# Performance work log

Hardware: AMD Instinct MI355X
Metric: run time of the kernel (lower is better)

## Reference

```python
import jax, jax.numpy as jnp
import numpy as np

B, L, H, E = 16, 1024, 8, 64
S, D = L, E
TOKEN_NUM = L


def setup_inputs() -> dict:
    key = jax.random.key(0)
    kq, kk, kv, kw = jax.random.split(key, 4)
    queries = jax.random.normal(kq, (B, L, H, E), dtype=jnp.float32)
    keys = jax.random.normal(kk, (B, S, H, E), dtype=jnp.float32)
    values = jax.random.normal(kv, (B, S, H, D), dtype=jnp.float32)
    # init as in module: eye + randn, shaped [1, num_heads=1, T, T]
    weight_mat = (jnp.eye(TOKEN_NUM, dtype=jnp.float32)
                  + jax.random.normal(kw, (TOKEN_NUM, TOKEN_NUM), dtype=jnp.float32))[None, None]
    tau = jnp.ones((1, 1, TOKEN_NUM, 1), dtype=jnp.float32)
    attn_mask = jnp.zeros((1,), dtype=bool)  # unused (mask_flag=False)
    return {"queries": queries, "keys": keys, "values": values,
            "weight_mat": weight_mat, "tau": tau, "attn_mask": attn_mask}


def reference(queries, keys, values, weight_mat, tau, attn_mask):
    # queries: [B,L,H,E], keys: [B,S,H,E], values: [B,S,H,D]
    scale = 1.0 / jnp.sqrt(jnp.asarray(queries.shape[-1], queries.dtype))
    scores = jnp.einsum('blhe,bshe->bhls', queries, keys) * scale  # [B,H,L,S]
    # learned modulation: softmax(weight_mat / softplus(tau)) over last dim
    w = jax.nn.softmax(weight_mat / jax.nn.softplus(tau), axis=-1)  # [1,1,L,S]
    A = jax.nn.softmax(scores * w, axis=-1)  # inside-softmax multiplicative path
    # dropout is identity in eval mode
    V = jnp.einsum('bhls,bshd->blhd', A, values)  # [B,L,H,D]
    return V
```

## Files before the change

kernel.cpp:

```cpp
#include <hip/hip_runtime.h>

using short8 = __attribute__((ext_vector_type(8))) short;
using f32x16 = __attribute__((ext_vector_type(16))) float;

__device__ __forceinline__ short b16(float f) {
  __bf16 h = (__bf16)f;
  return __builtin_bit_cast(short, h);
}
__device__ __forceinline__ short8 pack8(const float4& a, const float4& b) {
  short8 r;
  r[0] = b16(a.x); r[1] = b16(a.y); r[2] = b16(a.z); r[3] = b16(a.w);
  r[4] = b16(b.x); r[5] = b16(b.y); r[6] = b16(b.z); r[7] = b16(b.w);
  return r;
}
__device__ __forceinline__ unsigned pk2(float lo, float hi) {
  return ((unsigned)(unsigned short)b16(hi) << 16) | (unsigned)(unsigned short)b16(lo);
}

__global__ __launch_bounds__(256) void w_softmax_kernel(
    const float* __restrict__ wm, const float* __restrict__ tau,
    float* __restrict__ wout) {
  const int row = blockIdx.x;
  const int tid = threadIdx.x;
  const float sp  = log1pf(__expf(tau[row]));
  const float inv = 1.0f / sp;
  const float4* src = (const float4*)(wm + (size_t)row * 1024);
  float4 v = src[tid];
  float v0 = v.x * inv, v1 = v.y * inv, v2 = v.z * inv, v3 = v.w * inv;
  float mx = fmaxf(fmaxf(v0, v1), fmaxf(v2, v3));
  #pragma unroll
  for (int m = 1; m < 64; m <<= 1) mx = fmaxf(mx, __shfl_xor(mx, m));
  __shared__ float red[8];
  const int wv = tid >> 6;
  if ((tid & 63) == 0) red[wv] = mx;
  __syncthreads();
  mx = fmaxf(fmaxf(red[0], red[1]), fmaxf(red[2], red[3]));
  float e0 = __expf(v0 - mx), e1 = __expf(v1 - mx);
  float e2 = __expf(v2 - mx), e3 = __expf(v3 - mx);
  float s = e0 + e1 + e2 + e3;
  #pragma unroll
  for (int m = 1; m < 64; m <<= 1) s += __shfl_xor(s, m);
  if ((tid & 63) == 0) red[4 + wv] = s;
  __syncthreads();
  s = red[4] + red[5] + red[6] + red[7];
  const float r = 0.125f / s;
  float4* dst = (float4*)(wout + (size_t)row * 1024);
  float4 o; o.x = e0 * r; o.y = e1 * r; o.z = e2 * r; o.w = e3 * r;
  dst[tid] = o;
}

__global__ __launch_bounds__(256, 2) void attn_kernel(
    const float* __restrict__ Q, const float* __restrict__ K,
    const float* __restrict__ V, const float* __restrict__ W,
    float* __restrict__ O) {
  const int orig = blockIdx.x;
  const int bid  = (orig & 7) * 128 + (orig >> 3);
  const int qblk = bid >> 7;
  const int bh   = bid & 127;
  const int b = bh >> 3, h = bh & 7;

  const int tid = threadIdx.x, wv = tid >> 6, lane = tid & 63;
  const int ql = lane & 31, hi = lane >> 5;
  const int qg = qblk * 128 + wv * 32 + ql;

  __shared__ alignas(16) short Ks[2][4096];
  __shared__ alignas(16) short Vt[2][4096];
  __shared__ float Sc[128];

  const float* qrow = Q + ((size_t)(b * 1024 + qg)) * 512 + h * 64;
  short8 qb[4];
  #pragma unroll
  for (int es = 0; es < 4; ++es) {
    float4 f0 = *(const float4*)(qrow + es * 16 + hi * 8);
    float4 f1 = *(const float4*)(qrow + es * 16 + hi * 8 + 4);
    qb[es] = pack8(f0, f1);
  }

  const int srow = tid >> 2;
  const int cgrp = (tid & 3) * 16;
  const float* kp = K + ((size_t)(b * 1024 + srow)) * 512 + h * 64 + cgrp;
  const float* vp = V + ((size_t)(b * 1024 + srow)) * 512 + h * 64 + cgrp;
  const int kswz = (srow & 7) << 4;
  const int kwb0 = srow * 128 + ((cgrp * 2) ^ kswz);
  const int kwb1 = srow * 128 + ((cgrp * 2 + 16) ^ kswz);

  {
    float4 a0 = *(const float4*)(kp);
    float4 a1 = *(const float4*)(kp + 4);
    float4 a2 = *(const float4*)(kp + 8);
    float4 a3 = *(const float4*)(kp + 12);
    float4 c0 = *(const float4*)(vp);
    float4 c1 = *(const float4*)(vp + 4);
    float4 c2 = *(const float4*)(vp + 8);
    float4 c3 = *(const float4*)(vp + 12);
    *(short8*)((char*)Ks[0] + kwb0) = pack8(a0, a1);
    *(short8*)((char*)Ks[0] + kwb1) = pack8(a2, a3);
    float va[16] = {c0.x, c0.y, c0.z, c0.w, c1.x, c1.y, c1.z, c1.w,
                    c2.x, c2.y, c2.z, c2.w, c3.x, c3.y, c3.z, c3.w};
    #pragma unroll
    for (int j = 0; j < 16; ++j) {
      const int d = cgrp + j;
      const int vswz = (((d & 7) ^ (d >> 3)) & 7) << 4;
      *(short*)((char*)Vt[0] + d * 128 + ((srow * 2) ^ vswz)) = b16(va[j]);
    }
  }
  __syncthreads();

  f32x16 o0, o1;
  #pragma unroll
  for (int i = 0; i < 16; ++i) { o0[i] = 0.f; o1[i] = 0.f; }
  float m_r = -INFINITY, l_r = 0.f;

  const float* wr = W + (size_t)qg * 1024;

  #pragma unroll 1
  for (int kt = 0; kt < 16; ++kt) {
    const int c = kt & 1;
    const int s0 = kt * 64;

    float4 nk0, nk1, nk2, nk3, nv0, nv1, nv2, nv3;
    if (kt < 15) {
      const size_t soff = (size_t)((kt + 1) * 64) * 512;
      nk0 = *(const float4*)(kp + soff);      nk1 = *(const float4*)(kp + soff + 4);
      nk2 = *(const float4*)(kp + soff + 8);  nk3 = *(const float4*)(kp + soff + 12);
      nv0 = *(const float4*)(vp + soff);      nv1 = *(const float4*)(vp + soff + 4);
      nv2 = *(const float4*)(vp + soff + 8);  nv3 = *(const float4*)(vp + soff + 12);
    }

    float wreg[32];
    #pragma unroll
    for (int st = 0; st < 2; ++st)
      #pragma unroll
      for (int rg = 0; rg < 4; ++rg) {
        float4 t = *(const float4*)(wr + s0 + st * 32 + rg * 8 + hi * 4);
        wreg[st * 16 + rg * 4 + 0] = t.x;
        wreg[st * 16 + rg * 4 + 1] = t.y;
        wreg[st * 16 + rg * 4 + 2] = t.z;
        wreg[st * 16 + rg * 4 + 3] = t.w;
      }

    f32x16 sa0, sa1;
    #pragma unroll
    for (int i = 0; i < 16; ++i) { sa0[i] = 0.f; sa1[i] = 0.f; }
    {
      const int sr0 = ql, sr1 = 32 + ql;
      const char* kb0 = (const char*)Ks[c] + sr0 * 128;
      const char* kb1 = (const char*)Ks[c] + sr1 * 128;
      const int sz0 = (sr0 & 7) << 4, sz1 = (sr1 & 7) << 4;
      #pragma unroll
      for (int es = 0; es < 4; ++es) {
        short8 ka0 = *(const short8*)(kb0 + ((es * 32 + hi * 16) ^ sz0));
        short8 ka1 = *(const short8*)(kb1 + ((es * 32 + hi * 16) ^ sz1));
        sa0 = __builtin_amdgcn_mfma_f32_32x32x16_bf16(ka0, qb[es], sa0, 0, 0, 0);
        sa1 = __builtin_amdgcn_mfma_f32_32x32x16_bf16(ka1, qb[es], sa1, 0, 0, 0);
      }
    }

    float lg[32];
    #pragma unroll
    for (int reg = 0; reg < 16; ++reg) {
      lg[reg]      = sa0[reg] * wreg[reg];
      lg[16 + reg] = sa1[reg] * wreg[16 + reg];
    }

    float t16[16];
    #pragma unroll
    for (int i = 0; i < 16; ++i) t16[i] = fmaxf(lg[i], lg[i + 16]);
    float t8[8];
    #pragma unroll
    for (int i = 0; i < 8; ++i) t8[i] = fmaxf(t16[i], t16[i + 8]);
    float t4[4];
    #pragma unroll
    for (int i = 0; i < 4; ++i) t4[i] = fmaxf(t8[i], t8[i + 4]);
    float pmax = fmaxf(fmaxf(t4[0], t4[1]), fmaxf(t4[2], t4[3]));
    pmax = fmaxf(pmax, __shfl_xor(pmax, 32));

    if (!__all(pmax <= m_r + 8.0f)) {
      const float mnew = fmaxf(m_r, pmax);
      const float corr = __expf(m_r - mnew);
      m_r = mnew;
      l_r *= corr;
      if (lane < 32) Sc[wv * 32 + ql] = corr;
      #pragma unroll
      for (int reg = 0; reg < 16; ++reg) {
        const float cr = Sc[wv * 32 + ((reg & 3) + 8 * (reg >> 2) + 4 * hi)];
        o0[reg] *= cr; o1[reg] *= cr;
      }
    }

    float p[32];
    #pragma unroll
    for (int i = 0; i < 32; ++i) p[i] = __expf(lg[i] - m_r);
    float s16[16];
    #pragma unroll
    for (int i = 0; i < 16; ++i) s16[i] = p[i] + p[i + 16];
    float s8[8];
    #pragma unroll
    for (int i = 0; i < 8; ++i) s8[i] = s16[i] + s16[i + 8];
    float s4[4];
    #pragma unroll
    for (int i = 0; i < 4; ++i) s4[i] = s8[i] + s8[i + 4];
    float rs = (s4[0] + s4[1]) + (s4[2] + s4[3]);
    rs += __shfl_xor(rs, 32);
    l_r += rs;

    unsigned cc[16];
    #pragma unroll
    for (int t = 0; t < 16; ++t) cc[t] = pk2(p[2 * t], p[2 * t + 1]);
    short8 pa[4];
    #pragma unroll
    for (int ks = 0; ks < 4; ++ks) {
      unsigned snd0 = hi ? cc[4 * ks]     : cc[4 * ks + 2];
      unsigned snd1 = hi ? cc[4 * ks + 1] : cc[4 * ks + 3];
      unsigned e0 = __shfl_xor(snd0, 32);
      unsigned e1 = __shfl_xor(snd1, 32);
      uint4 dw;
      dw.x = hi ? e0 : cc[4 * ks];
      dw.y = hi ? e1 : cc[4 * ks + 1];
      dw.z = hi ? cc[4 * ks + 2] : e0;
      dw.w = hi ? cc[4 * ks + 3] : e1;
      pa[ks] = __builtin_bit_cast(short8, dw);
    }

    #pragma unroll
    for (int nt = 0; nt < 2; ++nt) {
      const int d = nt * 32 + ql;
      const char* vb = (const char*)Vt[c] + d * 128;
      const int vswz = (((d & 7) ^ (d >> 3)) & 7) << 4;
      #pragma unroll
      for (int ks = 0; ks < 4; ++ks) {
        short8 bf = *(const short8*)(vb + ((ks * 32 + hi * 16) ^ vswz));
        if (nt == 0) o0 = __builtin_amdgcn_mfma_f32_32x32x16_bf16(pa[ks], bf, o0, 0, 0, 0);
        else         o1 = __builtin_amdgcn_mfma_f32_32x32x16_bf16(pa[ks], bf, o1, 0, 0, 0);
      }
    }

    if (kt < 15) {
      *(short8*)((char*)Ks[c ^ 1] + kwb0) = pack8(nk0, nk1);
      *(short8*)((char*)Ks[c ^ 1] + kwb1) = pack8(nk2, nk3);
      float va[16] = {nv0.x, nv0.y, nv0.z, nv0.w, nv1.x, nv1.y, nv1.z, nv1.w,
                      nv2.x, nv2.y, nv2.z, nv2.w, nv3.x, nv3.y, nv3.z, nv3.w};
      #pragma unroll
      for (int j = 0; j < 16; ++j) {
        const int d = cgrp + j;
        const int vswz = (((d & 7) ^ (d >> 3)) & 7) << 4;
        *(short*)((char*)Vt[c ^ 1] + d * 128 + ((srow * 2) ^ vswz)) = b16(va[j]);
      }
    }
    __syncthreads();
  }

  if (lane < 32) Sc[wv * 32 + ql] = l_r;
  #pragma unroll
  for (int reg = 0; reg < 16; ++reg) {
    const int qq = (reg & 3) + 8 * (reg >> 2) + 4 * hi;
    const float lv = Sc[wv * 32 + qq];
    const float inv = 1.0f / lv;
    float* op = O + ((size_t)(b * 1024 + qblk * 128 + wv * 32 + qq)) * 512 + h * 64 + ql;
    op[0]  = o0[reg] * inv;
    op[32] = o1[reg] * inv;
  }
}

extern "C" void kernel_launch(void* const* d_in, const int* in_sizes, int n_in,
                              void* d_out, int out_size, void* d_ws, size_t ws_size,
                              hipStream_t stream) {
  const float* Q   = (const float*)d_in[0];
  const float* K   = (const float*)d_in[1];
  const float* V   = (const float*)d_in[2];
  const float* WM  = (const float*)d_in[3];
  const float* TAU = (const float*)d_in[4];
  float* Wbuf = (float*)d_ws;
  float* out  = (float*)d_out;

  w_softmax_kernel<<<dim3(1024), dim3(256), 0, stream>>>(WM, TAU, Wbuf);
  attn_kernel<<<dim3(1024), dim3(256), 0, stream>>>(Q, K, V, Wbuf, out);
}
```

Measured before the change: 254.7 us.

## Store modulation weights as transposed bf16, remap blocks per XCD, raise MFMA priority

The softmaxed weight matrix is now written in bf16 and a new kernel transposes it, so the attention kernel reads each score's weight as a 16-bit value from a column-major layout. The block-to-work mapping changes so every XCD handles 16 batch-heads across all query blocks, and s_setprio is raised around the MFMA sections. The intent is to halve the weight traffic and improve L2 locality of K/V per XCD. The costs are an extra kernel launch and bf16 rounding of the weights. Each lane now issues 32 scalar 2-byte loads strided by 1024 elements, which could coalesce poorly.

```diff
diff --git a/kernel.cpp b/kernel.cpp
--- a/kernel.cpp
+++ b/kernel.cpp
@@ -16,10 +16,13 @@
 __device__ __forceinline__ unsigned pk2(float lo, float hi) {
   return ((unsigned)(unsigned short)b16(hi) << 16) | (unsigned)(unsigned short)b16(lo);
 }
+__device__ __forceinline__ float bf2f(unsigned short u) {
+  return __builtin_bit_cast(float, ((unsigned)u) << 16);
+}
 
 __global__ __launch_bounds__(256) void w_softmax_kernel(
     const float* __restrict__ wm, const float* __restrict__ tau,
-    float* __restrict__ wout) {
+    unsigned short* __restrict__ wout) {
   const int row = blockIdx.x;
   const int tid = threadIdx.x;
   const float sp  = log1pf(__expf(tau[row]));
@@ -44,19 +47,44 @@
   __syncthreads();
   s = red[4] + red[5] + red[6] + red[7];
   const float r = 0.125f / s;
-  float4* dst = (float4*)(wout + (size_t)row * 1024);
-  float4 o; o.x = e0 * r; o.y = e1 * r; o.z = e2 * r; o.w = e3 * r;
-  dst[tid] = o;
+  ushort4 o;
+  o.x = (unsigned short)b16(e0 * r); o.y = (unsigned short)b16(e1 * r);
+  o.z = (unsigned short)b16(e2 * r); o.w = (unsigned short)b16(e3 * r);
+  *(ushort4*)(wout + (size_t)row * 1024 + tid * 4) = o;
+}
+
+__global__ __launch_bounds__(256) void w_transpose_kernel(
+    const unsigned short* __restrict__ win, unsigned short* __restrict__ wt) {
+  __shared__ unsigned short tile[64][73];
+  const int ti = blockIdx.x & 15;
+  const int tj = blockIdx.x >> 4;
+  const int t  = threadIdx.x;
+  const int qa = t >> 2;
+  const int sb = (t & 3) * 16;
+  const unsigned short* src = win + (size_t)(tj * 64 + qa) * 1024 + ti * 64 + sb;
+  short8 a0 = *(const short8*)(src);
+  short8 a1 = *(const short8*)(src + 8);
+  #pragma unroll
+  for (int j = 0; j < 8; ++j) { tile[qa][sb + j] = a0[j]; tile[qa][sb + 8 + j] = a1[j]; }
+  __syncthreads();
+  const int sr = t >> 2;
+  const int qb = (t & 3) * 16;
+  short8 w0, w1;
+  #pragma unroll
+  for (int j = 0; j < 8; ++j) { w0[j] = tile[qb + j][sr]; w1[j] = tile[qb + 8 + j][sr]; }
+  unsigned short* dst = wt + (size_t)(ti * 64 + sr) * 1024 + tj * 64 + qb;
+  *(short8*)(dst) = w0;
+  *(short8*)(dst + 8) = w1;
 }
 
 __global__ __launch_bounds__(256, 2) void attn_kernel(
     const float* __restrict__ Q, const float* __restrict__ K,
-    const float* __restrict__ V, const float* __restrict__ W,
+    const float* __restrict__ V, const unsigned short* __restrict__ Wt,
     float* __restrict__ O) {
   const int orig = blockIdx.x;
-  const int bid  = (orig & 7) * 128 + (orig >> 3);
-  const int qblk = bid >> 7;
-  const int bh   = bid & 127;
+  const int xcd  = orig & 7, slot = orig >> 3;
+  const int bh   = xcd * 16 + (slot >> 3);
+  const int qblk = slot & 7;
   const int b = bh >> 3, h = bh & 7;
 
   const int tid = threadIdx.x, wv = tid >> 6, lane = tid & 63;
@@ -111,7 +139,7 @@
   for (int i = 0; i < 16; ++i) { o0[i] = 0.f; o1[i] = 0.f; }
   float m_r = -INFINITY, l_r = 0.f;
 
-  const float* wr = W + (size_t)qg * 1024;
+  const unsigned short* wcol = Wt + qg;
 
   #pragma unroll 1
   for (int kt = 0; kt < 16; ++kt) {
@@ -127,17 +155,15 @@
       nv2 = *(const float4*)(vp + soff + 8);  nv3 = *(const float4*)(vp + soff + 12);
     }
 
-    float wreg[32];
+    unsigned short wu[32];
     #pragma unroll
     for (int st = 0; st < 2; ++st)
       #pragma unroll
-      for (int rg = 0; rg < 4; ++rg) {
-        float4 t = *(const float4*)(wr + s0 + st * 32 + rg * 8 + hi * 4);
-        wreg[st * 16 + rg * 4 + 0] = t.x;
-        wreg[st * 16 + rg * 4 + 1] = t.y;
-        wreg[st * 16 + rg * 4 + 2] = t.z;
-        wreg[st * 16 + rg * 4 + 3] = t.w;
-      }
+      for (int rg = 0; rg < 4; ++rg)
+        #pragma unroll
+        for (int cc = 0; cc < 4; ++cc)
+          wu[st * 16 + rg * 4 + cc] =
+              wcol[(size_t)(s0 + st * 32 + rg * 8 + 4 * hi + cc) * 1024];
 
     f32x16 sa0, sa1;
     #pragma unroll
@@ -147,6 +173,7 @@
       const char* kb0 = (const char*)Ks[c] + sr0 * 128;
       const char* kb1 = (const char*)Ks[c] + sr1 * 128;
       const int sz0 = (sr0 & 7) << 4, sz1 = (sr1 & 7) << 4;
+      __builtin_amdgcn_s_setprio(1);
       #pragma unroll
       for (int es = 0; es < 4; ++es) {
         short8 ka0 = *(const short8*)(kb0 + ((es * 32 + hi * 16) ^ sz0));
@@ -154,13 +181,14 @@
         sa0 = __builtin_amdgcn_mfma_f32_32x32x16_bf16(ka0, qb[es], sa0, 0, 0, 0);
         sa1 = __builtin_amdgcn_mfma_f32_32x32x16_bf16(ka1, qb[es], sa1, 0, 0, 0);
       }
+      __builtin_amdgcn_s_setprio(0);
     }
 
     float lg[32];
     #pragma unroll
     for (int reg = 0; reg < 16; ++reg) {
-      lg[reg]      = sa0[reg] * wreg[reg];
-      lg[16 + reg] = sa1[reg] * wreg[16 + reg];
+      lg[reg]      = sa0[reg] * bf2f(wu[reg]);
+      lg[16 + reg] = sa1[reg] * bf2f(wu[16 + reg]);
     }
 
     float t16[16];
@@ -204,24 +232,25 @@
     rs += __shfl_xor(rs, 32);
     l_r += rs;
 
-    unsigned cc[16];
-    #pragma unroll
-    for (int t = 0; t < 16; ++t) cc[t] = pk2(p[2 * t], p[2 * t + 1]);
+    unsigned cc16[16];
+    #pragma unroll
+    for (int t = 0; t < 16; ++t) cc16[t] = pk2(p[2 * t], p[2 * t + 1]);
     short8 pa[4];
     #pragma unroll
     for (int ks = 0; ks < 4; ++ks) {
-      unsigned snd0 = hi ? cc[4 * ks]     : cc[4 * ks + 2];
-      unsigned snd1 = hi ? cc[4 * ks + 1] : cc[4 * ks + 3];
+      unsigned snd0 = hi ? cc16[4 * ks]     : cc16[4 * ks + 2];
+      unsigned snd1 = hi ? cc16[4 * ks + 1] : cc16[4 * ks + 3];
       unsigned e0 = __shfl_xor(snd0, 32);
       unsigned e1 = __shfl_xor(snd1, 32);
       uint4 dw;
-      dw.x = hi ? e0 : cc[4 * ks];
-      dw.y = hi ? e1 : cc[4 * ks + 1];
-      dw.z = hi ? cc[4 * ks + 2] : e0;
-      dw.w = hi ? cc[4 * ks + 3] : e1;
+      dw.x = hi ? e0 : cc16[4 * ks];
+      dw.y = hi ? e1 : cc16[4 * ks + 1];
+      dw.z = hi ? cc16[4 * ks + 2] : e0;
+      dw.w = hi ? cc16[4 * ks + 3] : e1;
       pa[ks] = __builtin_bit_cast(short8, dw);
     }
 
+    __builtin_amdgcn_s_setprio(1);
     #pragma unroll
     for (int nt = 0; nt < 2; ++nt) {
       const int d = nt * 32 + ql;
@@ -234,6 +263,7 @@
         else         o1 = __builtin_amdgcn_mfma_f32_32x32x16_bf16(pa[ks], bf, o1, 0, 0, 0);
       }
     }
+    __builtin_amdgcn_s_setprio(0);
 
     if (kt < 15) {
       *(short8*)((char*)Ks[c ^ 1] + kwb0) = pack8(nk0, nk1);
@@ -270,9 +300,11 @@
   const float* V   = (const float*)d_in[2];
   const float* WM  = (const float*)d_in[3];
   const float* TAU = (const float*)d_in[4];
-  float* Wbuf = (float*)d_ws;
-  float* out  = (float*)d_out;
-
-  w_softmax_kernel<<<dim3(1024), dim3(256), 0, stream>>>(WM, TAU, Wbuf);
-  attn_kernel<<<dim3(1024), dim3(256), 0, stream>>>(Q, K, V, Wbuf, out);
-}
+  unsigned short* Wrm = (unsigned short*)d_ws;
+  unsigned short* Wt  = (unsigned short*)((char*)d_ws + (1 << 21));
+  float* out = (float*)d_out;
+
+  w_softmax_kernel<<<dim3(1024), dim3(256), 0, stream>>>(WM, TAU, Wrm);
+  w_transpose_kernel<<<dim3(256), dim3(256), 0, stream>>>(Wrm, Wt);
+  attn_kernel<<<dim3(1024), dim3(256), 0, stream>>>(Q, K, V, Wt, out);
+}
```

New measurement: 234.2 us. 1.09x faster.
